# Kernel optimization log

Hardware: AMD Instinct MI355X
Metric: run time of the kernel (lower is better)

Reference implementation:

```python
import jax, jax.numpy as jnp
import numpy as np

D_MODEL = 1024
H = 16
D_K = D_MODEL // H
WINDOW = 256
NEG = -1e9


def setup_inputs() -> dict:
    key = jax.random.key(0)
    ks = jax.random.split(key, 7)
    B, S = 2, 4096
    sc = 0.02
    return {
        "q": jax.random.normal(ks[0], (B, S, D_MODEL), jnp.float32),
        "k": jax.random.normal(ks[1], (B, S, D_MODEL), jnp.float32),
        "v": jax.random.normal(ks[2], (B, S, D_MODEL), jnp.float32),
        "wq": jax.random.normal(ks[3], (D_MODEL, D_MODEL), jnp.float32) * sc,
        "wk": jax.random.normal(ks[4], (D_MODEL, D_MODEL), jnp.float32) * sc,
        "wv": jax.random.normal(ks[5], (D_MODEL, D_MODEL), jnp.float32) * sc,
        "wo": jax.random.normal(ks[6], (D_MODEL, D_MODEL), jnp.float32) * sc,
    }


def _local_mask(seq_len: int, window_size: int):
    left = (window_size - 1) // 2
    right = window_size - 1 - left
    idx = jnp.arange(seq_len)
    dist = jnp.abs(idx[None, :] - idx[:, None])
    return (dist <= left) | (dist <= right)  # [S, S] bool


def reference(q, k, v, wq, wk, wv, wo):
    B, S, _ = q.shape
    # torch Linear: x @ W.T
    def proj(x, w):
        return (x @ w.T).reshape(B, S, H, D_K).transpose(0, 2, 1, 3)  # [B,H,S,Dk]
    Q, K, V = proj(q, wq), proj(k, wk), proj(v, wv)
    scores = jnp.einsum("bhqd,bhkd->bhqk", Q, K) / jnp.sqrt(jnp.float32(D_K))
    mask = _local_mask(S, WINDOW)
    scores = jnp.where(mask[None, None], scores, NEG)
    attn = jax.nn.softmax(scores, axis=-1)
    x = jnp.einsum("bhqk,bhkd->bhqd", attn, V)
    x = x.transpose(0, 2, 1, 3).reshape(B, S, D_MODEL)
    return x @ wo.T
```

## Files before the change

kernel.cpp:

```cpp
#include <hip/hip_runtime.h>
#include <hip/hip_bf16.h>

#define S_LEN 4096
#define B_SZ 2
#define DM 1024
#define NH 16
#define DH 64

typedef __attribute__((ext_vector_type(8))) short short8;
typedef __attribute__((ext_vector_type(4))) float f32x4;

__device__ __forceinline__ ushort f2b(float f) {
  union { __hip_bfloat16 b; ushort u; } cv;
  cv.b = __float2bfloat16(f);
  return cv.u;
}

__device__ __forceinline__ void glds16(const ushort* g, ushort* l) {
  __builtin_amdgcn_global_load_lds(
      (const __attribute__((address_space(1))) void*)g,
      (__attribute__((address_space(3))) void*)l, 16, 0, 0);
}

__global__ void cvt_all(const float* __restrict__ q, const float* __restrict__ k,
                        const float* __restrict__ v, const float* __restrict__ wq,
                        const float* __restrict__ wk, const float* __restrict__ wv,
                        const float* __restrict__ wo, ushort* __restrict__ dst) {
  const int NX4 = 2097152;
  const int NW4 = 262144;
  const int total = 3 * NX4 + 4 * NW4;
  for (int i = blockIdx.x * blockDim.x + threadIdx.x; i < total;
       i += gridDim.x * blockDim.x) {
    const float* s;
    int j;
    if (i < NX4) { s = q; j = i; }
    else if (i < 2 * NX4) { s = k; j = i - NX4; }
    else if (i < 3 * NX4) { s = v; j = i - 2 * NX4; }
    else {
      int t = i - 3 * NX4;
      int wsel = t >> 18;
      j = t & (NW4 - 1);
      s = wsel == 0 ? wq : wsel == 1 ? wk : wsel == 2 ? wv : wo;
    }
    float4 val = reinterpret_cast<const float4*>(s)[j];
    ushort4 o;
    o.x = f2b(val.x); o.y = f2b(val.y); o.z = f2b(val.z); o.w = f2b(val.w);
    reinterpret_cast<ushort4*>(dst)[i] = o;
  }
}

__device__ __forceinline__ short8 ldsrd(const ushort* base, int row, int cb) {
  const int pcb = cb ^ ((row & 7) << 4);
  return *reinterpret_cast<const short8*>(
      reinterpret_cast<const char*>(base) + row * 128 + pcb);
}

template <int MODE>
__launch_bounds__(512, 2)
__global__ void gemmP(const ushort* __restrict__ A0, const ushort* __restrict__ A1,
                      const ushort* __restrict__ A2, const ushort* __restrict__ W0,
                      const ushort* __restrict__ W1, const ushort* __restrict__ W2,
                      void* __restrict__ O0, void* __restrict__ O1,
                      void* __restrict__ O2) {
  __shared__ ushort As[3][16384];
  __shared__ ushort Bs[3][8192];
  const int tid = threadIdx.x;
  const int lane = tid & 63, w = tid >> 6;
  const int wm = w >> 1, wn = w & 1;
  const int g = lane >> 4, lr = lane & 15;
  const int m0 = blockIdx.x * 256;
  const int ysel = (MODE == 0) ? (blockIdx.y >> 3) : 0;
  const ushort* A = (MODE == 0) ? (ysel == 0 ? A0 : ysel == 1 ? A1 : A2) : A0;
  const ushort* W = (MODE == 0) ? (ysel == 0 ? W0 : ysel == 1 ? W1 : W2) : W0;
  const int n0 = ((MODE == 0) ? (blockIdx.y & 7) : blockIdx.y) * 128;

  const int row_r = tid >> 3;
  const int cb = ((tid & 7) * 16) ^ ((row_r & 7) << 4);
  const ushort* Asrc = A + (size_t)(m0 + row_r) * DM + (cb >> 1);
  const ushort* Wsrc = W + (size_t)(n0 + row_r) * DM + (cb >> 1);

#define STG_ALL(bs, kt)                                                      \
  { const int kq = (kt) * 64;                                                \
    glds16(Asrc + kq,                        &As[bs][w * 512]);              \
    glds16(Asrc + (size_t)64 * DM + kq,      &As[bs][4096 + w * 512]);       \
    glds16(Asrc + (size_t)128 * DM + kq,     &As[bs][8192 + w * 512]);       \
    glds16(Asrc + (size_t)192 * DM + kq,     &As[bs][12288 + w * 512]);      \
    glds16(Wsrc + kq,                        &Bs[bs][w * 512]);              \
    glds16(Wsrc + (size_t)64 * DM + kq,      &Bs[bs][4096 + w * 512]); }

  f32x4 acc[4][4] = {};
  short8 af[4][2], b0[2][2], b1[2][2];

  STG_ALL(0, 0);
  STG_ALL(1, 1);

  int bc = 0;
  for (int kt = 0; kt < 16; ++kt) {
    const int bs = bc >= 1 ? bc - 1 : bc + 2;
    const int tn = kt + 2 < 16 ? kt + 2 : 15;
    asm volatile("s_waitcnt vmcnt(6)" ::: "memory");
    __builtin_amdgcn_s_barrier();
    __builtin_amdgcn_sched_barrier(0);
    const ushort* Ab = &As[bc][0];
    const ushort* Bb = &Bs[bc][0];
#pragma unroll
    for (int m = 0; m < 4; m++)
#pragma unroll
      for (int kk = 0; kk < 2; kk++)
        af[m][kk] = ldsrd(Ab, wm * 64 + m * 16 + lr, kk * 64 + g * 16);
#pragma unroll
    for (int n = 0; n < 2; n++)
#pragma unroll
      for (int kk = 0; kk < 2; kk++) {
        b0[n][kk] = ldsrd(Bb, wn * 64 + n * 16 + lr, kk * 64 + g * 16);
        b1[n][kk] = ldsrd(Bb, wn * 64 + 32 + n * 16 + lr, kk * 64 + g * 16);
      }
    STG_ALL(bs, tn);
    __builtin_amdgcn_sched_barrier(0);
    asm volatile("s_waitcnt lgkmcnt(0)" ::: "memory");
    __builtin_amdgcn_sched_barrier(0);
    __builtin_amdgcn_s_setprio(1);
#pragma unroll
    for (int m = 0; m < 4; m++)
#pragma unroll
      for (int n = 0; n < 2; n++)
#pragma unroll
        for (int kk = 0; kk < 2; kk++)
          acc[m][n] = __builtin_amdgcn_mfma_f32_16x16x32_bf16(af[m][kk], b0[n][kk],
                                                              acc[m][n], 0, 0, 0);
#pragma unroll
    for (int m = 0; m < 4; m++)
#pragma unroll
      for (int n = 0; n < 2; n++)
#pragma unroll
        for (int kk = 0; kk < 2; kk++)
          acc[m][2 + n] = __builtin_amdgcn_mfma_f32_16x16x32_bf16(af[m][kk], b1[n][kk],
                                                                  acc[m][2 + n], 0, 0, 0);
    __builtin_amdgcn_s_setprio(0);
    __builtin_amdgcn_sched_barrier(0);
    bc = bc + 1 == 3 ? 0 : bc + 1;
  }
#undef STG_ALL

  const int colB = n0 + wn * 64;
#pragma unroll
  for (int m = 0; m < 4; ++m) {
    const int row0 = m0 + wm * 64 + m * 16 + g * 4;
#pragma unroll
    for (int n = 0; n < 4; ++n) {
      const int col = colB + n * 16 + lr;
      if (MODE == 2) {
#pragma unroll
        for (int r = 0; r < 4; r++)
          reinterpret_cast<float*>(O0)[(size_t)(row0 + r) * DM + col] = acc[m][n][r];
      } else if (ysel == 0 || ysel == 1) {
        ushort* O = reinterpret_cast<ushort*>(ysel == 0 ? O0 : O1);
#pragma unroll
        for (int r = 0; r < 4; r++)
          O[(size_t)(row0 + r) * DM + col] = f2b(acc[m][n][r]);
      } else {
        const int b = row0 >> 12, s0 = row0 & 4095;
        const int h = col >> 6, dk = col & 63;
        ushort4 o;
        o.x = f2b(acc[m][n][0]); o.y = f2b(acc[m][n][1]);
        o.z = f2b(acc[m][n][2]); o.w = f2b(acc[m][n][3]);
        *reinterpret_cast<ushort4*>(
            reinterpret_cast<ushort*>(O2) +
            (((size_t)(b * NH + h) * DH + dk) << 12) + s0) = o;
      }
    }
  }
}

__global__ void attn_local(const ushort* __restrict__ Qp, const ushort* __restrict__ Kp,
                           const ushort* __restrict__ Vt, ushort* __restrict__ Ao) {
  __shared__ ushort Ks[2][4096];
  __shared__ ushort Vs[2][4096];
  __shared__ ushort Ps[8][16 * 72];
  const int tid = threadIdx.x;
  const int lane = tid & 63;
  const int w = tid >> 6;
  const int g = lane >> 4, lr = lane & 15;
  const int bh = blockIdx.y, b = bh >> 4, h = bh & 15;
  const int q0 = blockIdx.x * 128;

  const float C_SCALE = 0.125f * 1.44269504f;
  const float C_M = 8.0f * 1.44269504f;

  const int qrow = q0 + w * 16 + lr;
  const ushort* qptr = Qp + ((size_t)b * S_LEN + qrow) * DM + h * DH;
  short8 qf[2];
  qf[0] = *reinterpret_cast<const short8*>(qptr + g * 8);
  qf[1] = *reinterpret_cast<const short8*>(qptr + 32 + g * 8);

  float l_r[4] = {0.f, 0.f, 0.f, 0.f};
  f32x4 acc_o[4] = {};

  const int sr = tid >> 3;
  const int scb = (tid & 7) * 16;

  const int t_lo = q0 >= 128 ? q0 - 128 : 0;
  const int t_hi = (q0 + 256) <= S_LEN ? (q0 + 256) : S_LEN;

#define STAGE(bb, kk0)                                                        \
  {                                                                           \
    const int cbk = scb ^ ((sr & 7) << 4);                                    \
    glds16(Kp + ((size_t)b * S_LEN + (kk0) + sr) * DM + h * DH + cbk / 2,     \
           &Ks[bb][w * 512]);                                                 \
    glds16(Vt + (((size_t)bh * DH + sr) << 12) + (kk0) + cbk / 2,             \
           &Vs[bb][w * 512]);                                                 \
  }

  STAGE(0, t_lo);

  int it = 0;
  for (int k0 = t_lo; k0 < t_hi; k0 += 64, ++it) {
    const int cur = it & 1;
    asm volatile("s_waitcnt vmcnt(0)" ::: "memory");
    __builtin_amdgcn_s_barrier();
    __builtin_amdgcn_sched_barrier(0);
    if (k0 + 64 < t_hi) STAGE(cur ^ 1, k0 + 64);
    __builtin_amdgcn_sched_barrier(0);

    f32x4 sc[4] = {};
#pragma unroll
    for (int kk = 0; kk < 2; kk++) {
#pragma unroll
      for (int nt = 0; nt < 4; nt++) {
        const int kr = nt * 16 + lr;
        const int cbk = (kk * 64 + g * 16) ^ ((kr & 7) << 4);
        short8 kf = *reinterpret_cast<const short8*>(
            reinterpret_cast<const char*>(&Ks[cur][0]) + kr * 128 + cbk);
        sc[nt] = __builtin_amdgcn_mfma_f32_16x16x32_bf16(qf[kk], kf, sc[nt], 0, 0, 0);
      }
    }
    const bool edge = (k0 < q0) || (k0 > q0 + 64);
    if (edge) {
#pragma unroll
      for (int nt = 0; nt < 4; nt++) {
        const int key = k0 + nt * 16 + lr;
#pragma unroll
        for (int r = 0; r < 4; r++) {
          const int qr = q0 + w * 16 + g * 4 + r;
          int d = qr - key; d = d < 0 ? -d : d;
          float arg = fmaf(sc[nt][r], C_SCALE, -C_M);
          arg = (d <= 128) ? arg : -400.f;
          const float p = exp2f(arg);
          sc[nt][r] = p;
          l_r[r] += p;
        }
      }
    } else {
#pragma unroll
      for (int nt = 0; nt < 4; nt++)
#pragma unroll
        for (int r = 0; r < 4; r++) {
          const float p = exp2f(fmaf(sc[nt][r], C_SCALE, -C_M));
          sc[nt][r] = p;
          l_r[r] += p;
        }
    }

    ushort* myP = Ps[w];
#pragma unroll
    for (int nt = 0; nt < 4; nt++)
#pragma unroll
      for (int r = 0; r < 4; r++)
        myP[(g * 4 + r) * 72 + nt * 16 + lr] = f2b(sc[nt][r]);
    asm volatile("s_waitcnt lgkmcnt(0)" ::: "memory");
    __builtin_amdgcn_sched_barrier(0);

#pragma unroll
    for (int kk = 0; kk < 2; kk++) {
      short8 pf2 = *reinterpret_cast<const short8*>(myP + lr * 72 + kk * 32 + g * 8);
#pragma unroll
      for (int nt = 0; nt < 4; nt++) {
        const int vr = nt * 16 + lr;
        const int cbk = (kk * 64 + g * 16) ^ ((vr & 7) << 4);
        short8 vf = *reinterpret_cast<const short8*>(
            reinterpret_cast<const char*>(&Vs[cur][0]) + vr * 128 + cbk);
        acc_o[nt] = __builtin_amdgcn_mfma_f32_16x16x32_bf16(pf2, vf, acc_o[nt], 0, 0, 0);
      }
    }
  }
#undef STAGE

  float inv[4];
#pragma unroll
  for (int r = 0; r < 4; r++) {
    float l = l_r[r];
    l += __shfl_xor(l, 1);
    l += __shfl_xor(l, 2);
    l += __shfl_xor(l, 4);
    l += __shfl_xor(l, 8);
    inv[r] = 1.0f / l;
  }
  const int qr0 = q0 + w * 16 + g * 4;
  ushort* orow = Ao + (size_t)b * S_LEN * DM + h * DH;
#pragma unroll
  for (int nt = 0; nt < 4; nt++)
#pragma unroll
    for (int r = 0; r < 4; r++)
      orow[(size_t)(qr0 + r) * DM + nt * 16 + lr] = f2b(acc_o[nt][r] * inv[r]);
}

extern "C" void kernel_launch(void* const* d_in, const int* in_sizes, int n_in,
                              void* d_out, int out_size, void* d_ws, size_t ws_size,
                              hipStream_t stream) {
  const float* q  = (const float*)d_in[0];
  const float* k  = (const float*)d_in[1];
  const float* v  = (const float*)d_in[2];
  const float* wq = (const float*)d_in[3];
  const float* wk = (const float*)d_in[4];
  const float* wv = (const float*)d_in[5];
  const float* wo = (const float*)d_in[6];

  const size_t NX = (size_t)B_SZ * S_LEN * DM;
  const size_t NW = (size_t)DM * DM;
  if (ws_size < (7 * NX + 4 * NW) * sizeof(ushort)) return;

  ushort* ws  = (ushort*)d_ws;
  ushort* qb  = ws;
  ushort* kb  = qb + NX;
  ushort* vb  = kb + NX;
  ushort* wqb = vb + NX;
  ushort* wkb = wqb + NW;
  ushort* wvb = wkb + NW;
  ushort* wob = wvb + NW;
  ushort* Qp  = wob + NW;
  ushort* Kp  = Qp + NX;
  ushort* Vt  = Kp + NX;
  ushort* Ao  = Vt + NX;

  cvt_all<<<dim3(2048), dim3(256), 0, stream>>>(q, k, v, wq, wk, wv, wo, ws);

  gemmP<0><<<dim3(32, 24), dim3(512), 0, stream>>>(qb, kb, vb, wqb, wkb, wvb,
                                                   Qp, Kp, Vt);

  attn_local<<<dim3(32, 32), dim3(512), 0, stream>>>(Qp, Kp, Vt, Ao);

  gemmP<2><<<dim3(32, 8), dim3(512), 0, stream>>>(Ao, Ao, Ao, wob, wob, wob,
                                                  d_out, d_out, d_out);
}
```

Measured before the change: 150.6 us.

## Add 256x256-tile QKV projection GEMM with 4-stage BK=32 pipeline

Replaces the QKV projection GEMM with a new kernel. It uses 256x256 output tiles instead of 256x128, a K step of 32 and a 4-buffer LDS ring fed by direct global-to-LDS loads, and it issues the next stage's loads while the current stage's MFMAs run. The larger tile halves the grid from 768 to 384 blocks and is meant to raise operand reuse and hide load latency. The cost is more accumulator registers per thread, fewer blocks to balance across CUs, and 32-byte-wide LDS rows with a different swizzle.

```diff
diff --git a/kernel.cpp b/kernel.cpp
--- a/kernel.cpp
+++ b/kernel.cpp
@@ -54,6 +54,104 @@
   return *reinterpret_cast<const short8*>(
       reinterpret_cast<const char*>(base) + row * 128 + pcb);
 }
+__device__ __forceinline__ short8 ldsrd32(const ushort* base, int row, int cb) {
+  const int pcb = cb ^ ((row & 3) << 4);
+  return *reinterpret_cast<const short8*>(
+      reinterpret_cast<const char*>(base) + row * 64 + pcb);
+}
+
+__launch_bounds__(512, 2)
+__global__ void gemmQ(const ushort* __restrict__ A0, const ushort* __restrict__ A1,
+                      const ushort* __restrict__ A2, const ushort* __restrict__ W0,
+                      const ushort* __restrict__ W1, const ushort* __restrict__ W2,
+                      ushort* __restrict__ O0, ushort* __restrict__ O1,
+                      ushort* __restrict__ O2) {
+  __shared__ ushort As[4][8192];
+  __shared__ ushort Bs[4][8192];
+  const int tid = threadIdx.x;
+  const int lane = tid & 63, w = tid >> 6;
+  const int wm = w >> 2, wn = w & 3;
+  const int g = lane >> 4, lr = lane & 15;
+  const int m0 = blockIdx.x * 256;
+  const int ysel = blockIdx.y >> 2;
+  const ushort* A = ysel == 0 ? A0 : ysel == 1 ? A1 : A2;
+  const ushort* W = ysel == 0 ? W0 : ysel == 1 ? W1 : W2;
+  const int n0 = (blockIdx.y & 3) * 256;
+
+  const int srow = tid >> 2;
+  const int scb = ((tid & 3) * 16) ^ ((srow & 3) << 4);
+  const ushort* Asrc = A + (size_t)(m0 + srow) * DM + (scb >> 1);
+  const ushort* Wsrc = W + (size_t)(n0 + srow) * DM + (scb >> 1);
+
+#define STGQ(bs, kt)                                                         \
+  { const int kq = (kt) * 32;                                                \
+    glds16(Asrc + kq,                     &As[bs][w * 512]);                 \
+    glds16(Asrc + (size_t)128 * DM + kq,  &As[bs][4096 + w * 512]);          \
+    glds16(Wsrc + kq,                     &Bs[bs][w * 512]);                 \
+    glds16(Wsrc + (size_t)128 * DM + kq,  &Bs[bs][4096 + w * 512]); }
+
+  f32x4 acc[8][4] = {};
+  short8 af[8], bf[4];
+
+  STGQ(0, 0);
+  STGQ(1, 1);
+  STGQ(2, 2);
+
+  for (int kt = 0; kt < 32; ++kt) {
+    const int bc = kt & 3;
+    const int bs = (kt + 3) & 3;
+    const int tn = kt + 3 < 32 ? kt + 3 : 31;
+    asm volatile("s_waitcnt vmcnt(8)" ::: "memory");
+    __builtin_amdgcn_s_barrier();
+    __builtin_amdgcn_sched_barrier(0);
+    const ushort* Ab = &As[bc][0];
+    const ushort* Bb = &Bs[bc][0];
+#pragma unroll
+    for (int m = 0; m < 8; m++)
+      af[m] = ldsrd32(Ab, wm * 128 + m * 16 + lr, g * 16);
+#pragma unroll
+    for (int n = 0; n < 4; n++)
+      bf[n] = ldsrd32(Bb, wn * 64 + n * 16 + lr, g * 16);
+    STGQ(bs, tn);
+    __builtin_amdgcn_sched_barrier(0);
+    asm volatile("s_waitcnt lgkmcnt(0)" ::: "memory");
+    __builtin_amdgcn_sched_barrier(0);
+    __builtin_amdgcn_s_setprio(1);
+#pragma unroll
+    for (int m = 0; m < 8; m++)
+#pragma unroll
+      for (int n = 0; n < 4; n++)
+        acc[m][n] = __builtin_amdgcn_mfma_f32_16x16x32_bf16(af[m], bf[n],
+                                                            acc[m][n], 0, 0, 0);
+    __builtin_amdgcn_s_setprio(0);
+    __builtin_amdgcn_sched_barrier(0);
+  }
+#undef STGQ
+
+  const int colB = n0 + wn * 64;
+#pragma unroll
+  for (int m = 0; m < 8; ++m) {
+    const int row0 = m0 + wm * 128 + m * 16 + g * 4;
+#pragma unroll
+    for (int n = 0; n < 4; ++n) {
+      const int col = colB + n * 16 + lr;
+      if (ysel == 0 || ysel == 1) {
+        ushort* O = ysel == 0 ? O0 : O1;
+#pragma unroll
+        for (int r = 0; r < 4; r++)
+          O[(size_t)(row0 + r) * DM + col] = f2b(acc[m][n][r]);
+      } else {
+        const int b = row0 >> 12, s0 = row0 & 4095;
+        const int h = col >> 6, dk = col & 63;
+        ushort4 o;
+        o.x = f2b(acc[m][n][0]); o.y = f2b(acc[m][n][1]);
+        o.z = f2b(acc[m][n][2]); o.w = f2b(acc[m][n][3]);
+        *reinterpret_cast<ushort4*>(
+            O2 + (((size_t)(b * NH + h) * DH + dk) << 12) + s0) = o;
+      }
+    }
+  }
+}
 
 template <int MODE>
 __launch_bounds__(512, 2)
@@ -334,8 +432,8 @@
 
   cvt_all<<<dim3(2048), dim3(256), 0, stream>>>(q, k, v, wq, wk, wv, wo, ws);
 
-  gemmP<0><<<dim3(32, 24), dim3(512), 0, stream>>>(qb, kb, vb, wqb, wkb, wvb,
-                                                   Qp, Kp, Vt);
+  gemmQ<<<dim3(32, 12), dim3(512), 0, stream>>>(qb, kb, vb, wqb, wkb, wvb,
+                                                Qp, Kp, Vt);
 
   attn_local<<<dim3(32, 32), dim3(512), 0, stream>>>(Qp, Kp, Vt, Ao);
 
```

New measurement: 159.0 us. 1.06x slower.
